# Performance work log

Measured on AMD Instinct MI355X. Metric: run time of the kernel, lower is better.

The kernel has to match this reference:

```python
import jax, jax.numpy as jnp
import numpy as np

MATCH_IOU = 0.5
IGNORE_IOU = 0.4
BOX_VARIANCE = jnp.asarray([0.1, 0.1, 0.2, 0.2], dtype=jnp.float32)
BACKGROUND_CLASS = -1.0
IGNORE_CLASS = -2.0

M_ANCHORS = 76725  # RetinaNet P3-P7 on 640x640, 9 anchors/loc
BATCH = 16
N_GT = 100
NUM_CLASSES = 20


def setup_inputs() -> dict:
    key = jax.random.key(0)
    k1, k2, k3, k4, k5 = jax.random.split(key, 5)
    # anchors in xywh (top-left x, y, width, height)
    axy = jax.random.uniform(k1, (M_ANCHORS, 2), minval=0.0, maxval=600.0)
    awh = jax.random.uniform(k2, (M_ANCHORS, 2), minval=16.0, maxval=256.0)
    anchor_boxes = jnp.concatenate([axy, awh], axis=-1).astype(jnp.float32)
    # gt boxes [B, N, 5] = [x, y, w, h, class_id] in xywh
    gxy = jax.random.uniform(k3, (BATCH, N_GT, 2), minval=0.0, maxval=600.0)
    gwh = jax.random.uniform(k4, (BATCH, N_GT, 2), minval=8.0, maxval=200.0)
    gcls = jax.random.randint(k5, (BATCH, N_GT, 1), 0, NUM_CLASSES).astype(jnp.float32)
    gt_boxes = jnp.concatenate([gxy, gwh, gcls], axis=-1)
    return {"anchor_boxes": anchor_boxes, "gt_boxes": gt_boxes}


def _xywh_to_corners(b):
    x, y, w, h = b[..., 0], b[..., 1], b[..., 2], b[..., 3]
    return x, y, x + w, y + h


def _pairwise_iou(anchors, gt):
    # anchors: [M, 4], gt: [B, N, 4] -> iou: [B, M, N]
    ax1, ay1, ax2, ay2 = _xywh_to_corners(anchors)          # [M]
    gx1, gy1, gx2, gy2 = _xywh_to_corners(gt)               # [B, N]
    ax1 = ax1[None, :, None]; ay1 = ay1[None, :, None]
    ax2 = ax2[None, :, None]; ay2 = ay2[None, :, None]
    gx1 = gx1[:, None, :]; gy1 = gy1[:, None, :]
    gx2 = gx2[:, None, :]; gy2 = gy2[:, None, :]
    iw = jnp.maximum(jnp.minimum(ax2, gx2) - jnp.maximum(ax1, gx1), 0.0)
    ih = jnp.maximum(jnp.minimum(ay2, gy2) - jnp.maximum(ay1, gy1), 0.0)
    inter = iw * ih                                          # [B, M, N]
    a_area = (anchors[:, 2] * anchors[:, 3])[None, :, None]
    g_area = (gt[..., 2] * gt[..., 3])[:, None, :]
    union = a_area + g_area - inter
    return jnp.where(union > 0.0, inter / union, 0.0)


def reference(anchor_boxes, gt_boxes):
    # anchor_boxes: [M, 4] xywh; gt_boxes: [B, N, 5] xywh + class
    gt_xywh = gt_boxes[..., :4]
    cls_ids = gt_boxes[..., 4]                               # [B, N]

    iou = _pairwise_iou(anchor_boxes, gt_xywh)               # [B, M, N]
    max_iou = jnp.max(iou, axis=-1)                          # [B, M]
    matched_gt_idx = jnp.argmax(iou, axis=-1)                # [B, M]
    positive_mask = max_iou >= MATCH_IOU
    negative_mask = max_iou < IGNORE_IOU
    ignore_mask = jnp.logical_not(positive_mask | negative_mask)

    # gather matched gt boxes / classes: [B, M, 5]
    matched = jnp.take_along_axis(gt_boxes, matched_gt_idx[..., None], axis=1)
    mx, my, mw, mh = matched[..., 0], matched[..., 1], matched[..., 2], matched[..., 3]
    matched_cls = matched[..., 4]

    # encode xywh -> center deltas, scaled by variance
    acx = anchor_boxes[:, 0] + 0.5 * anchor_boxes[:, 2]
    acy = anchor_boxes[:, 1] + 0.5 * anchor_boxes[:, 3]
    aw = anchor_boxes[:, 2]
    ah = anchor_boxes[:, 3]
    gcx = mx + 0.5 * mw
    gcy = my + 0.5 * mh
    box_target = jnp.stack(
        [
            (gcx - acx[None, :]) / aw[None, :],
            (gcy - acy[None, :]) / ah[None, :],
            jnp.log(mw / aw[None, :]),
            jnp.log(mh / ah[None, :]),
        ],
        axis=-1,
    ) / BOX_VARIANCE                                          # [B, M, 4]

    cls_target = jnp.where(positive_mask, matched_cls, BACKGROUND_CLASS)
    cls_target = jnp.where(ignore_mask, IGNORE_CLASS, cls_target)

    label = jnp.concatenate([box_target, cls_target[..., None]], axis=-1)  # [B, M, 5]
    any_nan = jnp.any(jnp.isnan(label), axis=-1, keepdims=True)
    label = jnp.where(any_nan, IGNORE_CLASS, label)
    return label
```

## Files before the change

### kernel.cpp

```cpp
#include <hip/hip_runtime.h>
#include <math.h>

#define M_ANCHORS 76725
#define BATCH     16
#define N_GT      100
#define HALF_GT   50
#define MATCH_IOU  0.5f
#define IGNORE_IOU 0.4f

__global__ __launch_bounds__(256) void retina_encode_kernel(
    const float* __restrict__ anchors,
    const float* __restrict__ gt,
    float* __restrict__ out)
{
#pragma clang fp contract(off)
    __shared__ float4 s_box[N_GT];
    __shared__ float  s_ga[N_GT];
    __shared__ float  s_raw[N_GT * 5];

    const int b = blockIdx.y;
    const int t = threadIdx.x;
    const int a = blockIdx.x * 128 + (t >> 1);
    const int half = t & 1;

    for (int i = t; i < N_GT * 5; i += blockDim.x)
        s_raw[i] = gt[b * (N_GT * 5) + i];
    __syncthreads();
    if (t < N_GT) {
        const float gx = s_raw[t * 5 + 0];
        const float gy = s_raw[t * 5 + 1];
        const float gw = s_raw[t * 5 + 2];
        const float gh = s_raw[t * 5 + 3];
        s_box[t] = make_float4(gx, gy, gx + gw, gy + gh);
        s_ga[t]  = gw * gh;
    }
    __syncthreads();

    if (a >= M_ANCHORS) return;

    const float4 av = *reinterpret_cast<const float4*>(anchors + (size_t)a * 4);
    const float ax1 = av.x, ay1 = av.y, aw = av.z, ah = av.w;
    const float ax2 = ax1 + aw;
    const float ay2 = ay1 + ah;
    const float aarea = aw * ah;

    const int jbase = half ? HALF_GT : 0;

    float bI = 0.0f;
    float bS = 1.0f;
    int   bj = jbase;
    bool  flag = false;

    #pragma unroll 10
    for (int jj = 0; jj < HALF_GT; ++jj) {
        const int j = jbase + jj;
        const float4 g = s_box[j];
        float iw = fmaxf(fminf(ax2, g.z) - fmaxf(ax1, g.x), 0.0f);
        float ih = fminf(ay2, g.w) - fmaxf(ay1, g.y);
        const float inter = iw * ih;
        const float S   = aarea + s_ga[j];
        const float pb  = bI * S;
        const float d   = fmaf(inter, bS, -pb);
        const float tol = fmaf(4e-6f, pb, -1e-33f);
        flag = flag | (fabsf(d) <= tol);
        if (d > 0.0f) { bI = inter; bS = S; bj = j; }
    }

    const float oI = __shfl_xor(bI, 1);
    const float oS = __shfl_xor(bS, 1);
    const int   oj = __shfl_xor(bj, 1);
    const int   of = __shfl_xor((int)flag, 1);

    if (half) return;

    bool anyflag = flag | (of != 0);
    const float pA = oI * bS;
    const float pB = bI * oS;
    const float dd = pA - pB;
    const float ptol = fmaf(4e-6f, fmaxf(pA, pB), -1e-33f);
    anyflag = anyflag | (fabsf(dd) <= ptol);

    float BI = bI, BS = bS;
    int   bidx = bj;
    if (dd > 0.0f) { BI = oI; BS = oS; bidx = oj; }

    float M;
    if (!anyflag) {
        M = BI / (BS - BI);
    } else {
        float best = -1.0f;
        bidx = 0;
        for (int j = 0; j < N_GT; ++j) {
            const float4 g = s_box[j];
            float iw = fmaxf(fminf(ax2, g.z) - fmaxf(ax1, g.x), 0.0f);
            float ih = fmaxf(fminf(ay2, g.w) - fmaxf(ay1, g.y), 0.0f);
            const float inter = iw * ih;
            const float uni = (aarea + s_ga[j]) - inter;
            const float iou = (uni > 0.0f) ? (inter / uni) : 0.0f;
            if (iou > best) { best = iou; bidx = j; }
        }
        M = best;
    }

    const float mx   = s_raw[bidx * 5 + 0];
    const float my   = s_raw[bidx * 5 + 1];
    const float mw   = s_raw[bidx * 5 + 2];
    const float mh   = s_raw[bidx * 5 + 3];
    const float mcls = s_raw[bidx * 5 + 4];

    const float acx = ax1 + 0.5f * aw;
    const float acy = ay1 + 0.5f * ah;
    const float gcx = mx + 0.5f * mw;
    const float gcy = my + 0.5f * mh;

    float t0 = ((gcx - acx) / aw) / 0.1f;
    float t1 = ((gcy - acy) / ah) / 0.1f;
    float t2 = logf(mw / aw) / 0.2f;
    float t3 = logf(mh / ah) / 0.2f;

    const bool pos = (M >= MATCH_IOU);
    const bool neg = (M < IGNORE_IOU);
    float cls = pos ? mcls : -1.0f;
    if (!pos && !neg) cls = -2.0f;

    if (isnan(t0) || isnan(t1) || isnan(t2) || isnan(t3) || isnan(cls)) {
        t0 = t1 = t2 = t3 = cls = -2.0f;
    }

    float* o = out + ((size_t)b * M_ANCHORS + a) * 5;
    o[0] = t0;
    o[1] = t1;
    o[2] = t2;
    o[3] = t3;
    o[4] = cls;
}

extern "C" void kernel_launch(void* const* d_in, const int* in_sizes, int n_in,
                              void* d_out, int out_size, void* d_ws, size_t ws_size,
                              hipStream_t stream) {
    const float* anchors = (const float*)d_in[0];
    const float* gt      = (const float*)d_in[1];
    float* out           = (float*)d_out;

    const dim3 block(256, 1, 1);
    const dim3 grid((M_ANCHORS + 127) / 128, BATCH, 1);
    retina_encode_kernel<<<grid, block, 0, stream>>>(anchors, gt, out);
}
```

Measured before the change: 76.58 us.

## Use one thread per anchor instead of splitting GT scan across thread pairs

Each anchor is now handled by a single thread that scans all 100 GT boxes, fully unrolled. This removes the pairwise shuffle merge and the idle second half during the encode stage. Blocks shrink to 128 threads, and the variance divisions become multiplications by reciprocal constants. The trade-off is half as many threads, each with a longer serial dependency chain in the argmax loop. Multiplying by 10 or 5 instead of dividing by 0.1 or 0.2 may change low bits of the result.

```diff
diff --git a/kernel.cpp b/kernel.cpp
--- a/kernel.cpp
+++ b/kernel.cpp
@@ -4,11 +4,10 @@
 #define M_ANCHORS 76725
 #define BATCH     16
 #define N_GT      100
-#define HALF_GT   50
 #define MATCH_IOU  0.5f
 #define IGNORE_IOU 0.4f
 
-__global__ __launch_bounds__(256) void retina_encode_kernel(
+__global__ __launch_bounds__(128) void retina_encode_kernel(
     const float* __restrict__ anchors,
     const float* __restrict__ gt,
     float* __restrict__ out)
@@ -20,10 +19,9 @@
 
     const int b = blockIdx.y;
     const int t = threadIdx.x;
-    const int a = blockIdx.x * 128 + (t >> 1);
-    const int half = t & 1;
+    const int a = blockIdx.x * 128 + t;
 
-    for (int i = t; i < N_GT * 5; i += blockDim.x)
+    for (int i = t; i < N_GT * 5; i += 128)
         s_raw[i] = gt[b * (N_GT * 5) + i];
     __syncthreads();
     if (t < N_GT) {
@@ -44,19 +42,16 @@
     const float ay2 = ay1 + ah;
     const float aarea = aw * ah;
 
-    const int jbase = half ? HALF_GT : 0;
-
     float bI = 0.0f;
     float bS = 1.0f;
-    int   bj = jbase;
+    int   bj = 0;
     bool  flag = false;
 
-    #pragma unroll 10
-    for (int jj = 0; jj < HALF_GT; ++jj) {
-        const int j = jbase + jj;
+    #pragma unroll
+    for (int j = 0; j < N_GT; ++j) {
         const float4 g = s_box[j];
-        float iw = fmaxf(fminf(ax2, g.z) - fmaxf(ax1, g.x), 0.0f);
-        float ih = fminf(ay2, g.w) - fmaxf(ay1, g.y);
+        const float iw = fmaxf(fminf(ax2, g.z) - fmaxf(ax1, g.x), 0.0f);
+        const float ih = fminf(ay2, g.w) - fmaxf(ay1, g.y);
         const float inter = iw * ih;
         const float S   = aarea + s_ga[j];
         const float pb  = bI * S;
@@ -66,34 +61,18 @@
         if (d > 0.0f) { bI = inter; bS = S; bj = j; }
     }
 
-    const float oI = __shfl_xor(bI, 1);
-    const float oS = __shfl_xor(bS, 1);
-    const int   oj = __shfl_xor(bj, 1);
-    const int   of = __shfl_xor((int)flag, 1);
-
-    if (half) return;
-
-    bool anyflag = flag | (of != 0);
-    const float pA = oI * bS;
-    const float pB = bI * oS;
-    const float dd = pA - pB;
-    const float ptol = fmaf(4e-6f, fmaxf(pA, pB), -1e-33f);
-    anyflag = anyflag | (fabsf(dd) <= ptol);
-
-    float BI = bI, BS = bS;
-    int   bidx = bj;
-    if (dd > 0.0f) { BI = oI; BS = oS; bidx = oj; }
-
     float M;
-    if (!anyflag) {
-        M = BI / (BS - BI);
+    int bidx = bj;
+    if (!flag) {
+        M = bI / (bS - bI);
     } else {
         float best = -1.0f;
         bidx = 0;
+        #pragma unroll 1
         for (int j = 0; j < N_GT; ++j) {
             const float4 g = s_box[j];
-            float iw = fmaxf(fminf(ax2, g.z) - fmaxf(ax1, g.x), 0.0f);
-            float ih = fmaxf(fminf(ay2, g.w) - fmaxf(ay1, g.y), 0.0f);
+            const float iw = fmaxf(fminf(ax2, g.z) - fmaxf(ax1, g.x), 0.0f);
+            const float ih = fmaxf(fminf(ay2, g.w) - fmaxf(ay1, g.y), 0.0f);
             const float inter = iw * ih;
             const float uni = (aarea + s_ga[j]) - inter;
             const float iou = (uni > 0.0f) ? (inter / uni) : 0.0f;
@@ -113,10 +92,10 @@
     const float gcx = mx + 0.5f * mw;
     const float gcy = my + 0.5f * mh;
 
-    float t0 = ((gcx - acx) / aw) / 0.1f;
-    float t1 = ((gcy - acy) / ah) / 0.1f;
-    float t2 = logf(mw / aw) / 0.2f;
-    float t3 = logf(mh / ah) / 0.2f;
+    float t0 = ((gcx - acx) / aw) * 10.0f;
+    float t1 = ((gcy - acy) / ah) * 10.0f;
+    float t2 = logf(mw / aw) * 5.0f;
+    float t3 = logf(mh / ah) * 5.0f;
 
     const bool pos = (M >= MATCH_IOU);
     const bool neg = (M < IGNORE_IOU);
@@ -142,7 +121,7 @@
     const float* gt      = (const float*)d_in[1];
     float* out           = (float*)d_out;
 
-    const dim3 block(256, 1, 1);
+    const dim3 block(128, 1, 1);
     const dim3 grid((M_ANCHORS + 127) / 128, BATCH, 1);
     retina_encode_kernel<<<grid, block, 0, stream>>>(anchors, gt, out);
 }
```

New measurement: 77.16 us. No clear change (+0.8%).
